# Optimization experiments

Measured on AMD Instinct MI355X. Metric: run time of the kernel, lower is better.

The kernel has to match this reference:

```python
import jax, jax.numpy as jnp
import numpy as np

B, H, S, D = 2, 16, 2048, 64


def setup_inputs() -> dict:
    key = jax.random.key(0)
    kq, kk, kv, km = jax.random.split(key, 4)
    q = jax.random.normal(kq, (B, H, S, D), dtype=jnp.float32)
    k = jax.random.normal(kk, (B, H, S, D), dtype=jnp.float32)
    v = jax.random.normal(kv, (B, H, S, D), dtype=jnp.float32)
    mask = jax.random.uniform(km, (B, H, S, S), dtype=jnp.float32)
    return {"q": q, "k": k, "v": v, "mask": mask}


def reference(q, k, v, mask):
    # qk: [B,H,S,S]
    qk = jnp.einsum("bhqd,bhkd->bhqk", q, k)
    qkm = qk * mask
    # abs-sum-clamp normalizer; original uses .detach() -> stop_gradient
    r = jnp.sum(jnp.abs(qkm), axis=-1, keepdims=True)
    r = jnp.maximum(jax.lax.stop_gradient(r), 1.0)
    o = jnp.einsum("bhqk,bhkd->bhqd", qkm / r, v)
    return o
```

## Files before the change

### kernel.cpp

```cpp
#include <hip/hip_runtime.h>

#define S_LEN 2048
#define DHEAD 64
#define TQ 64
#define TK 64
#define NIT (S_LEN / TK)
#define BH 32

typedef __attribute__((ext_vector_type(4))) short short4v;
typedef __attribute__((ext_vector_type(8))) short short8v;
typedef __attribute__((ext_vector_type(4))) float float4v;
typedef __attribute__((ext_vector_type(2))) int int2v;
typedef __attribute__((ext_vector_type(4))) int int4v;

__device__ __forceinline__ unsigned bfr(float x) {
    return __builtin_bit_cast(unsigned, x) + 0x8000u;
}
__device__ __forceinline__ int packbf(float a, float b) {
    return (int)((bfr(a) >> 16) | (bfr(b) & 0xFFFF0000u));
}

__global__ __launch_bounds__(256, 4)
void fra_kernel(const float* __restrict__ qg, const float* __restrict__ kg,
                const float* __restrict__ vg, const float* __restrict__ mg,
                float* __restrict__ og) {
    const int tid = threadIdx.x;
    const int l  = tid & 63;
    const int w  = tid >> 6;
    const int lg = l >> 4;
    const int ln = l & 15;
    const int qt = blockIdx.x;
    const int bh = blockIdx.y;
    const int q0 = qt * TQ;

    __shared__ __align__(16) short Kt[64 * 72];
    __shared__ __align__(16) short Vt[64 * 72];
    __shared__ float Mt[64 * 65];

    const float* qbase = qg + (size_t)bh * S_LEN * DHEAD;
    const float* kbase = kg + (size_t)bh * S_LEN * DHEAD;
    const float* vbase = vg + (size_t)bh * S_LEN * DHEAD;
    const float* mbase = mg + (size_t)bh * S_LEN * S_LEN + (size_t)q0 * S_LEN;
    float*       obase = og + (size_t)bh * S_LEN * DHEAD;

    const int qrow = q0 + 16 * w + ln;
    short4v qf[4];
    #pragma unroll
    for (int s = 0; s < 4; ++s) {
        float4v qv = *(const float4v*)(qbase + (size_t)qrow * DHEAD + 16 * s + 4 * lg);
        int2v t; t.x = packbf(qv.x, qv.y); t.y = packbf(qv.z, qv.w);
        qf[s] = __builtin_bit_cast(short4v, t);
    }

    float4v oacc[4] = {{0.f,0.f,0.f,0.f},{0.f,0.f,0.f,0.f},
                       {0.f,0.f,0.f,0.f},{0.f,0.f,0.f,0.f}};
    float rpart = 0.f;

    const int sr = tid >> 4;
    const int sc = (tid & 15) * 4;

    for (int it = 0; it < NIT; ++it) {
        const int k0 = it * TK;

        float4v kv[4], mv[4];
        #pragma unroll
        for (int p = 0; p < 4; ++p) {
            kv[p] = *(const float4v*)(kbase + (size_t)(k0 + sr + 16 * p) * DHEAD + sc);
            mv[p] = *(const float4v*)(mbase + (size_t)(sr + 16 * p) * S_LEN + k0 + sc);
        }
        float vv[16];
        #pragma unroll
        for (int i = 0; i < 16; ++i)
            vv[i] = vbase[(size_t)(k0 + 16 * w + i) * DHEAD + l];

        __syncthreads();

        #pragma unroll
        for (int p = 0; p < 4; ++p) {
            int2v t; t.x = packbf(kv[p].x, kv[p].y); t.y = packbf(kv[p].z, kv[p].w);
            *(short4v*)&Kt[(sr + 16 * p) * 72 + sc] = __builtin_bit_cast(short4v, t);
            float* mrow = &Mt[(sr + 16 * p) * 65 + sc];
            mrow[0] = mv[p].x; mrow[1] = mv[p].y; mrow[2] = mv[p].z; mrow[3] = mv[p].w;
        }
        {
            int4v t0, t1;
            t0.x = packbf(vv[0], vv[1]);   t0.y = packbf(vv[2], vv[3]);
            t0.z = packbf(vv[4], vv[5]);   t0.w = packbf(vv[6], vv[7]);
            t1.x = packbf(vv[8], vv[9]);   t1.y = packbf(vv[10], vv[11]);
            t1.z = packbf(vv[12], vv[13]); t1.w = packbf(vv[14], vv[15]);
            *(short8v*)&Vt[l * 72 + 16 * w]     = __builtin_bit_cast(short8v, t0);
            *(short8v*)&Vt[l * 72 + 16 * w + 8] = __builtin_bit_cast(short8v, t1);
        }
        __syncthreads();

        #pragma unroll
        for (int mt = 0; mt < 4; ++mt) {
            float4v c1 = {0.f, 0.f, 0.f, 0.f};
            #pragma unroll
            for (int s = 0; s < 4; ++s) {
                short4v a1 = *(const short4v*)&Kt[(16 * mt + ln) * 72 + 16 * s + 4 * lg];
                c1 = __builtin_amdgcn_mfma_f32_16x16x16bf16_1k(a1, qf[s], c1, 0, 0, 0);
            }
            const float* mrow = &Mt[(16 * w + ln) * 65 + 16 * mt + 4 * lg];
            float p0 = c1.x * mrow[0];
            float p1 = c1.y * mrow[1];
            float p2 = c1.z * mrow[2];
            float p3 = c1.w * mrow[3];
            rpart += fabsf(p0) + fabsf(p1) + fabsf(p2) + fabsf(p3);
            int2v t; t.x = packbf(p0, p1); t.y = packbf(p2, p3);
            short4v a2 = __builtin_bit_cast(short4v, t);
            #pragma unroll
            for (int nt = 0; nt < 4; ++nt) {
                short4v b2 = *(const short4v*)&Vt[(16 * nt + ln) * 72 + 16 * mt + 4 * lg];
                oacc[nt] = __builtin_amdgcn_mfma_f32_16x16x16bf16_1k(a2, b2, oacc[nt], 0, 0, 0);
            }
        }
    }

    float r = rpart;
    r += __shfl_xor(r, 16);
    r += __shfl_xor(r, 32);

    #pragma unroll
    for (int reg = 0; reg < 4; ++reg) {
        float rq  = __shfl(r, 4 * lg + reg);
        float inv = 1.0f / fmaxf(rq, 1.0f);
        const int orow = q0 + 16 * w + 4 * lg + reg;
        #pragma unroll
        for (int nt = 0; nt < 4; ++nt) {
            obase[(size_t)orow * DHEAD + 16 * nt + ln] = oacc[nt][reg] * inv;
        }
    }
}

extern "C" void kernel_launch(void* const* d_in, const int* in_sizes, int n_in,
                              void* d_out, int out_size, void* d_ws, size_t ws_size,
                              hipStream_t stream) {
    const float* q = (const float*)d_in[0];
    const float* k = (const float*)d_in[1];
    const float* v = (const float*)d_in[2];
    const float* m = (const float*)d_in[3];
    float* o = (float*)d_out;
    (void)in_sizes; (void)n_in; (void)out_size; (void)d_ws; (void)ws_size;
    dim3 grid(S_LEN / TQ, BH);
    fra_kernel<<<grid, dim3(256, 1, 1), 0, stream>>>(q, k, v, m, o);
}
```

Baseline: 753.5 us.

## Load mask directly into registers, double-buffer prefetch, remap workgroups across XCDs

The mask is now read straight from global memory into registers in MFMA fragment layout with nontemporal loads, which removes the shared-memory mask tile. K, V and mask for the next key tile are prefetched into registers while the current tile's MFMAs run, using an unrolled ping-pong of two mask register buffers. Workgroup IDs are remapped so consecutive heads land on the same XCD for L2 reuse of K/V, and output stores are nontemporal. This adds register pressure, and the per-lane mask loads are 16-byte row-strided, which may coalesce less well than the old tile loads.

```diff
diff --git a/kernel.cpp b/kernel.cpp
--- a/kernel.cpp
+++ b/kernel.cpp
@@ -6,6 +6,8 @@
 #define TK 64
 #define NIT (S_LEN / TK)
 #define BH 32
+#define NWG ((S_LEN / TQ) * BH)
+#define NXCD 8
 
 typedef __attribute__((ext_vector_type(4))) short short4v;
 typedef __attribute__((ext_vector_type(8))) short short8v;
@@ -20,6 +22,68 @@
     return (int)((bfr(a) >> 16) | (bfr(b) & 0xFFFF0000u));
 }
 
+#define FRA_BODY(IT, MCUR, MNEXT)                                              \
+    {                                                                          \
+        _Pragma("unroll")                                                      \
+        for (int p = 0; p < 4; ++p) {                                          \
+            int2v t; t.x = packbf(kv[p].x, kv[p].y);                           \
+            t.y = packbf(kv[p].z, kv[p].w);                                    \
+            *(short4v*)&Kt[(sr + 16 * p) * 72 + sc] =                          \
+                __builtin_bit_cast(short4v, t);                                \
+        }                                                                      \
+        {                                                                      \
+            int4v t0, t1;                                                      \
+            t0.x = packbf(vv[0], vv[1]);   t0.y = packbf(vv[2], vv[3]);        \
+            t0.z = packbf(vv[4], vv[5]);   t0.w = packbf(vv[6], vv[7]);        \
+            t1.x = packbf(vv[8], vv[9]);   t1.y = packbf(vv[10], vv[11]);      \
+            t1.z = packbf(vv[12], vv[13]); t1.w = packbf(vv[14], vv[15]);      \
+            *(short8v*)&Vt[l * 72 + 16 * w]     = __builtin_bit_cast(short8v, t0); \
+            *(short8v*)&Vt[l * 72 + 16 * w + 8] = __builtin_bit_cast(short8v, t1); \
+        }                                                                      \
+        __syncthreads();                                                       \
+        {                                                                      \
+            const int kpf = ((IT) + 1 < NIT) ? ((IT) + 1) * TK : 0;            \
+            _Pragma("unroll")                                                  \
+            for (int p = 0; p < 4; ++p)                                        \
+                kv[p] = *(const float4v*)(kbase +                              \
+                    (size_t)(kpf + sr + 16 * p) * DHEAD + sc);                 \
+            _Pragma("unroll")                                                  \
+            for (int i = 0; i < 16; ++i)                                       \
+                vv[i] = vbase[(size_t)(kpf + 16 * w + i) * DHEAD + l];         \
+            const float* mp = mrow + kpf + 4 * lg;                             \
+            _Pragma("unroll")                                                  \
+            for (int mt = 0; mt < 4; ++mt)                                     \
+                MNEXT[mt] = __builtin_nontemporal_load(                        \
+                    (const float4v*)(mp + 16 * mt));                           \
+        }                                                                      \
+        _Pragma("unroll")                                                      \
+        for (int mt = 0; mt < 4; ++mt) {                                       \
+            float4v c1 = {0.f, 0.f, 0.f, 0.f};                                 \
+            _Pragma("unroll")                                                  \
+            for (int s = 0; s < 4; ++s) {                                      \
+                short4v a1 = *(const short4v*)&Kt[(16 * mt + ln) * 72 +        \
+                                                  16 * s + 4 * lg];            \
+                c1 = __builtin_amdgcn_mfma_f32_16x16x16bf16_1k(a1, qf[s], c1,  \
+                                                               0, 0, 0);       \
+            }                                                                  \
+            float p0 = c1.x * MCUR[mt].x;                                      \
+            float p1 = c1.y * MCUR[mt].y;                                      \
+            float p2 = c1.z * MCUR[mt].z;                                      \
+            float p3 = c1.w * MCUR[mt].w;                                      \
+            rpart += fabsf(p0) + fabsf(p1) + fabsf(p2) + fabsf(p3);            \
+            int2v t; t.x = packbf(p0, p1); t.y = packbf(p2, p3);               \
+            short4v a2 = __builtin_bit_cast(short4v, t);                       \
+            _Pragma("unroll")                                                  \
+            for (int nt = 0; nt < 4; ++nt) {                                   \
+                short4v b2 = *(const short4v*)&Vt[(16 * nt + ln) * 72 +        \
+                                                  16 * mt + 4 * lg];           \
+                oacc[nt] = __builtin_amdgcn_mfma_f32_16x16x16bf16_1k(          \
+                    a2, b2, oacc[nt], 0, 0, 0);                                \
+            }                                                                  \
+        }                                                                      \
+        __syncthreads();                                                       \
+    }
+
 __global__ __launch_bounds__(256, 4)
 void fra_kernel(const float* __restrict__ qg, const float* __restrict__ kg,
                 const float* __restrict__ vg, const float* __restrict__ mg,
@@ -29,18 +93,20 @@
     const int w  = tid >> 6;
     const int lg = l >> 4;
     const int ln = l & 15;
-    const int qt = blockIdx.x;
-    const int bh = blockIdx.y;
+
+    const int wgid = ((int)blockIdx.x % NXCD) * (NWG / NXCD) + (int)blockIdx.x / NXCD;
+    const int qt = wgid & 31;
+    const int bh = wgid >> 5;
     const int q0 = qt * TQ;
 
     __shared__ __align__(16) short Kt[64 * 72];
     __shared__ __align__(16) short Vt[64 * 72];
-    __shared__ float Mt[64 * 65];
 
     const float* qbase = qg + (size_t)bh * S_LEN * DHEAD;
     const float* kbase = kg + (size_t)bh * S_LEN * DHEAD;
     const float* vbase = vg + (size_t)bh * S_LEN * DHEAD;
-    const float* mbase = mg + (size_t)bh * S_LEN * S_LEN + (size_t)q0 * S_LEN;
+    const float* mrow  = mg + (size_t)bh * S_LEN * S_LEN
+                            + (size_t)(q0 + 16 * w + ln) * S_LEN;
     float*       obase = og + (size_t)bh * S_LEN * DHEAD;
 
     const int qrow = q0 + 16 * w + ln;
@@ -59,62 +125,24 @@
     const int sr = tid >> 4;
     const int sc = (tid & 15) * 4;
 
-    for (int it = 0; it < NIT; ++it) {
-        const int k0 = it * TK;
+    float4v kv[4];
+    float   vv[16];
+    float4v ma[4], mb[4];
 
-        float4v kv[4], mv[4];
-        #pragma unroll
-        for (int p = 0; p < 4; ++p) {
-            kv[p] = *(const float4v*)(kbase + (size_t)(k0 + sr + 16 * p) * DHEAD + sc);
-            mv[p] = *(const float4v*)(mbase + (size_t)(sr + 16 * p) * S_LEN + k0 + sc);
-        }
-        float vv[16];
-        #pragma unroll
-        for (int i = 0; i < 16; ++i)
-            vv[i] = vbase[(size_t)(k0 + 16 * w + i) * DHEAD + l];
+    #pragma unroll
+    for (int p = 0; p < 4; ++p)
+        kv[p] = *(const float4v*)(kbase + (size_t)(sr + 16 * p) * DHEAD + sc);
+    #pragma unroll
+    for (int i = 0; i < 16; ++i)
+        vv[i] = vbase[(size_t)(16 * w + i) * DHEAD + l];
+    #pragma unroll
+    for (int mt = 0; mt < 4; ++mt)
+        ma[mt] = __builtin_nontemporal_load(
+            (const float4v*)(mrow + 16 * mt + 4 * lg));
 
-        __syncthreads();
-
-        #pragma unroll
-        for (int p = 0; p < 4; ++p) {
-            int2v t; t.x = packbf(kv[p].x, kv[p].y); t.y = packbf(kv[p].z, kv[p].w);
-            *(short4v*)&Kt[(sr + 16 * p) * 72 + sc] = __builtin_bit_cast(short4v, t);
-            float* mrow = &Mt[(sr + 16 * p) * 65 + sc];
-            mrow[0] = mv[p].x; mrow[1] = mv[p].y; mrow[2] = mv[p].z; mrow[3] = mv[p].w;
-        }
-        {
-            int4v t0, t1;
-            t0.x = packbf(vv[0], vv[1]);   t0.y = packbf(vv[2], vv[3]);
-            t0.z = packbf(vv[4], vv[5]);   t0.w = packbf(vv[6], vv[7]);
-            t1.x = packbf(vv[8], vv[9]);   t1.y = packbf(vv[10], vv[11]);
-            t1.z = packbf(vv[12], vv[13]); t1.w = packbf(vv[14], vv[15]);
-            *(short8v*)&Vt[l * 72 + 16 * w]     = __builtin_bit_cast(short8v, t0);
-            *(short8v*)&Vt[l * 72 + 16 * w + 8] = __builtin_bit_cast(short8v, t1);
-        }
-        __syncthreads();
-
-        #pragma unroll
-        for (int mt = 0; mt < 4; ++mt) {
-            float4v c1 = {0.f, 0.f, 0.f, 0.f};
-            #pragma unroll
-            for (int s = 0; s < 4; ++s) {
-                short4v a1 = *(const short4v*)&Kt[(16 * mt + ln) * 72 + 16 * s + 4 * lg];
-                c1 = __builtin_amdgcn_mfma_f32_16x16x16bf16_1k(a1, qf[s], c1, 0, 0, 0);
-            }
-            const float* mrow = &Mt[(16 * w + ln) * 65 + 16 * mt + 4 * lg];
-            float p0 = c1.x * mrow[0];
-            float p1 = c1.y * mrow[1];
-            float p2 = c1.z * mrow[2];
-            float p3 = c1.w * mrow[3];
-            rpart += fabsf(p0) + fabsf(p1) + fabsf(p2) + fabsf(p3);
-            int2v t; t.x = packbf(p0, p1); t.y = packbf(p2, p3);
-            short4v a2 = __builtin_bit_cast(short4v, t);
-            #pragma unroll
-            for (int nt = 0; nt < 4; ++nt) {
-                short4v b2 = *(const short4v*)&Vt[(16 * nt + ln) * 72 + 16 * mt + 4 * lg];
-                oacc[nt] = __builtin_amdgcn_mfma_f32_16x16x16bf16_1k(a2, b2, oacc[nt], 0, 0, 0);
-            }
-        }
+    for (int itp = 0; itp < NIT; itp += 2) {
+        FRA_BODY(itp,     ma, mb)
+        FRA_BODY(itp + 1, mb, ma)
     }
 
     float r = rpart;
@@ -128,7 +156,8 @@
         const int orow = q0 + 16 * w + 4 * lg + reg;
         #pragma unroll
         for (int nt = 0; nt < 4; ++nt) {
-            obase[(size_t)orow * DHEAD + 16 * nt + ln] = oacc[nt][reg] * inv;
+            __builtin_nontemporal_store(oacc[nt][reg] * inv,
+                &obase[(size_t)orow * DHEAD + 16 * nt + ln]);
         }
     }
 }
@@ -142,6 +171,5 @@
     const float* m = (const float*)d_in[3];
     float* o = (float*)d_out;
     (void)in_sizes; (void)n_in; (void)out_size; (void)d_ws; (void)ws_size;
-    dim3 grid(S_LEN / TQ, BH);
-    fra_kernel<<<grid, dim3(256, 1, 1), 0, stream>>>(q, k, v, m, o);
+    fra_kernel<<<dim3(NWG), dim3(256, 1, 1), 0, stream>>>(q, k, v, m, o);
 }
```

After: 764.6 us. Within noise of the previous version (+1.5%).
